# Performance work log

Measured on AMD Instinct MI355X. Metric: run time of the kernel, lower is better.

## Reference

```python
import jax, jax.numpy as jnp
import numpy as np

N, E, B = 40000, 640000, 256
F_IN, H, D = 128, 128, 128  # num_node_features, hidden_dim, last_dim
EPS = 1e-5


def sage_conv(x, src, dst, Wl, bl, Wr, num_nodes):
    # PyG SAGEConv (mean aggr): out = lin_l(mean_j x_j) + lin_r(x)
    msg = x[src]                                            # [E, d] gather
    agg = jax.ops.segment_sum(msg, dst, num_segments=num_nodes)
    cnt = jax.ops.segment_sum(jnp.ones((src.shape[0],), x.dtype), dst,
                              num_segments=num_nodes)
    mean = agg / jnp.maximum(cnt, 1.0)[:, None]
    return mean @ Wl.T + bl + x @ Wr.T


def bn_eval(x, g, b, rm, rv):
    return g * (x - rm) * jax.lax.rsqrt(rv + EPS) + b


def lstm_cell(inp, h, c, Wih, Whh, bih, bhh):
    gates = inp @ Wih.T + h @ Whh.T + bih + bhh             # [B, 4D]
    i, f, g, o = jnp.split(gates, 4, axis=-1)
    c = jax.nn.sigmoid(f) * c + jax.nn.sigmoid(i) * jnp.tanh(g)
    h = jax.nn.sigmoid(o) * jnp.tanh(c)
    return h, c


def set2set(x, batch, Wih, Whh, bih, bhh, num_graphs, steps=3):
    d = x.shape[1]
    q_star = jnp.zeros((num_graphs, 2 * d), x.dtype)
    h = jnp.zeros((num_graphs, d), x.dtype)
    c = jnp.zeros((num_graphs, d), x.dtype)
    for _ in range(steps):
        h, c = lstm_cell(q_star, h, c, Wih, Whh, bih, bhh)
        q = h                                               # [B, D]
        e = jnp.sum(x * q[batch], axis=-1)                  # [N]
        emax = jax.ops.segment_max(e, batch, num_segments=num_graphs)
        a = jnp.exp(e - emax[batch])
        denom = jax.ops.segment_sum(a, batch, num_segments=num_graphs)
        a = a / denom[batch]
        r = jax.ops.segment_sum(a[:, None] * x, batch, num_segments=num_graphs)
        q_star = jnp.concatenate([q, r], axis=-1)
    return q_star


def setup_inputs() -> dict:
    key = jax.random.key(0)
    ks = jax.random.split(key, 20)
    x = jax.random.normal(ks[0], (N, F_IN), jnp.float32)
    edge_index = jax.random.randint(ks[1], (2, E), 0, N)
    batch = jnp.sort(jax.random.randint(ks[2], (N,), 0, B))
    s1, s2, sd = 1.0 / np.sqrt(F_IN), 1.0 / np.sqrt(H), 1.0 / np.sqrt(D)
    return {
        "x": x, "edge_index": edge_index, "batch": batch,
        "W1l": jax.random.normal(ks[3], (H, F_IN)) * s1,
        "b1l": jnp.zeros((H,)),
        "W1r": jax.random.normal(ks[4], (H, F_IN)) * s1,
        "g1": jnp.ones((H,)), "beta1": jnp.zeros((H,)),
        "rm1": jax.random.normal(ks[5], (H,)) * 0.1,
        "rv1": jax.random.uniform(ks[6], (H,), minval=0.5, maxval=1.5),
        "W2l": jax.random.normal(ks[7], (D, H)) * s2,
        "b2l": jnp.zeros((D,)),
        "W2r": jax.random.normal(ks[8], (D, H)) * s2,
        "g2": jnp.ones((D,)), "beta2": jnp.zeros((D,)),
        "rm2": jax.random.normal(ks[9], (D,)) * 0.1,
        "rv2": jax.random.uniform(ks[10], (D,), minval=0.5, maxval=1.5),
        "Wih": jax.random.normal(ks[11], (4 * D, 2 * D)) * sd,
        "Whh": jax.random.normal(ks[12], (4 * D, D)) * sd,
        "bih": jnp.zeros((4 * D,)), "bhh": jnp.zeros((4 * D,)),
        "Wp": jax.random.normal(ks[13], (D, 2 * D)) * sd,
        "bp": jnp.zeros((D,)),
    }


def reference(x, edge_index, batch, W1l, b1l, W1r, g1, beta1, rm1, rv1,
              W2l, b2l, W2r, g2, beta2, rm2, rv2, Wih, Whh, bih, bhh, Wp, bp):
    src, dst = edge_index[0], edge_index[1]
    num_nodes = x.shape[0]
    h1 = jax.nn.relu(bn_eval(sage_conv(x, src, dst, W1l, b1l, W1r, num_nodes),
                             g1, beta1, rm1, rv1))
    # dropout is identity in eval mode
    h2 = jax.nn.relu(bn_eval(sage_conv(h1, src, dst, W2l, b2l, W2r, num_nodes),
                             g2, beta2, rm2, rv2))
    q_star = set2set(h2, batch, Wih, Whh, bih, bhh, B, steps=3)  # [B, 2D]
    return q_star @ Wp.T + bp                                    # [B, D]
```

## Files before the change

kernel.cpp:

```cpp
#include <hip/hip_runtime.h>
#include <hip/hip_bf16.h>
#include <math.h>

#define NN 40000
#define NE 640000
#define NG 256
#define FD 128
#define SLOT 96
#define NBK 1000
#define NPB 40
#define ECAP 832
#define BPAD 32

typedef __attribute__((ext_vector_type(8))) short bf16x8;
typedef __attribute__((ext_vector_type(4))) float f32x4;

__device__ __forceinline__ float sigf(float x) { return 1.f / (1.f + __expf(-x)); }
__device__ __forceinline__ unsigned short f2b(float f) {
    unsigned int u = __float_as_uint(f);
    return (unsigned short)((u + 0x7FFFu + ((u >> 16) & 1u)) >> 16);
}
__device__ __forceinline__ float b2f(unsigned int u16) {
    return __uint_as_float(u16 << 16);
}

__global__ __launch_bounds__(256) void k_fused1(
    const float* __restrict__ A,
    const float* __restrict__ W1l, const float* __restrict__ W1r,
    unsigned short* __restrict__ C,
    const int* __restrict__ ei, const int* __restrict__ batch,
    int* __restrict__ gptr, int* __restrict__ bcnt, unsigned int* __restrict__ ebuf,
    const float* __restrict__ W2l, const float* __restrict__ W2r,
    unsigned short* __restrict__ Wb,
    const float* __restrict__ Wihf, const float* __restrict__ Whhf,
    unsigned short* __restrict__ Wb2)
{
    __shared__ unsigned short Ws[128 * 128];
    int bid = blockIdx.x, t = threadIdx.x;

    if ((bid < 2012) && (bid & 1)) {
        int sidx = bid >> 1;
        if (sidx < 625) {
            int i = sidx * 256 + t;
            int4 s4 = ((const int4*)ei)[i];
            int4 d4 = ((const int4*)(ei + NE))[i];
            int b0 = d4.x / NPB;
            int p0 = atomicAdd(&bcnt[b0 * BPAD], 1);
            if (p0 < ECAP) ebuf[b0 * ECAP + p0] =
                (unsigned int)s4.x | ((unsigned int)(d4.x - b0 * NPB) << 16);
            int b1 = d4.y / NPB;
            int p1 = atomicAdd(&bcnt[b1 * BPAD], 1);
            if (p1 < ECAP) ebuf[b1 * ECAP + p1] =
                (unsigned int)s4.y | ((unsigned int)(d4.y - b1 * NPB) << 16);
            int b2 = d4.z / NPB;
            int p2 = atomicAdd(&bcnt[b2 * BPAD], 1);
            if (p2 < ECAP) ebuf[b2 * ECAP + p2] =
                (unsigned int)s4.z | ((unsigned int)(d4.z - b2 * NPB) << 16);
            int b3 = d4.w / NPB;
            int p3 = atomicAdd(&bcnt[b3 * BPAD], 1);
            if (p3 < ECAP) ebuf[b3 * ECAP + p3] =
                (unsigned int)s4.w | ((unsigned int)(d4.w - b3 * NPB) << 16);
        } else if (sidx < 782) {
            int i = (sidx - 625) * 256 + t;
            if (i >= NN) return;
            int b = batch[i];
            int pb = (i == 0) ? -1 : batch[i - 1];
            for (int g = pb + 1; g <= b; g++) gptr[g] = i;
            if (i == NN - 1)
                for (int g = b + 1; g <= NG; g++) gptr[g] = NN;
        } else if (sidx < 814) {
            int j4 = (sidx - 782) * 256 + t;
            int seg = j4 >> 12, off4 = j4 & 4095;
            const float* W = seg ? W2r : W2l;
            float4 v = ((const float4*)W)[off4];
            ushort4 o;
            o.x = f2b(v.x); o.y = f2b(v.y); o.z = f2b(v.z); o.w = f2b(v.w);
            *(ushort4*)(Wb + (size_t)j4 * 4) = o;
        } else {
            int j4 = (sidx - 814) * 256 + t;
            float4 v;
            size_t off;
            if (j4 < 32768) {
                int r = j4 >> 6, f4 = j4 & 63;
                int c = f4 >> 1, h = f4 & 1;
                v = ((const float4*)Wihf)[j4];
                off = ((size_t)c * 512 + r) * 8 + h * 4;
            } else {
                int jj = j4 - 32768;
                int r = jj >> 5, f4 = jj & 31;
                int c = f4 >> 1, h = f4 & 1;
                v = ((const float4*)Whhf)[jj];
                off = (size_t)512 * 256 + ((size_t)c * 512 + r) * 8 + h * 4;
            }
            ushort4 o;
            o.x = f2b(v.x); o.y = f2b(v.y); o.z = f2b(v.z); o.w = f2b(v.w);
            *(ushort4*)(Wb2 + off) = o;
        }
        return;
    }

    int mblk2 = (bid < 2012) ? (bid >> 1) : (bid - 1006);
    int nh = mblk2 & 1;
    int mblk = mblk2 >> 1;
    {
        const float* Wsrc = nh ? W1r : W1l;
#pragma unroll
        for (int i = 0; i < 8; i++) {
            int f = i * 256 + t;
            int row = f >> 4, c = f & 15;
            float4 u0 = *(const float4*)(Wsrc + row * 128 + c * 8);
            float4 u1 = *(const float4*)(Wsrc + row * 128 + c * 8 + 4);
            unsigned short tmp[8];
            tmp[0] = f2b(u0.x); tmp[1] = f2b(u0.y); tmp[2] = f2b(u0.z); tmp[3] = f2b(u0.w);
            tmp[4] = f2b(u1.x); tmp[5] = f2b(u1.y); tmp[6] = f2b(u1.z); tmp[7] = f2b(u1.w);
            int cs = c ^ (row & 15);
            *(uint4*)&Ws[row * 128 + cs * 8] = *(const uint4*)tmp;
        }
    }
    __syncthreads();
    int w = t >> 6, lane = t & 63;
    int ln = lane & 15, quad = lane >> 4;
    int m0 = mblk * 64 + w * 16;
    bf16x8 a[4];
    {
        const float* Arow = A + (size_t)(m0 + ln) * 128;
#pragma unroll
        for (int ks = 0; ks < 4; ks++) {
            float4 u0 = *(const float4*)(Arow + ks * 32 + quad * 8);
            float4 u1 = *(const float4*)(Arow + ks * 32 + quad * 8 + 4);
            unsigned short tmp[8];
            tmp[0] = f2b(u0.x); tmp[1] = f2b(u0.y); tmp[2] = f2b(u0.z); tmp[3] = f2b(u0.w);
            tmp[4] = f2b(u1.x); tmp[5] = f2b(u1.y); tmp[6] = f2b(u1.z); tmp[7] = f2b(u1.w);
            a[ks] = *(const bf16x8*)tmp;
        }
    }
    for (int nt = 0; nt < 8; nt++) {
        int n0 = nt * 16;
        int row = n0 + ln;
        f32x4 acc = {0.f, 0.f, 0.f, 0.f};
#pragma unroll
        for (int ks = 0; ks < 4; ks++) {
            int c = ks * 4 + quad;
            bf16x8 b = *(const bf16x8*)&Ws[row * 128 + (c ^ (row & 15)) * 8];
            acc = __builtin_amdgcn_mfma_f32_16x16x32_bf16(a[ks], b, acc, 0, 0, 0);
        }
        size_t base = (size_t)(m0 + quad * 4) * 256 + nh * 128 + n0 + ln;
#pragma unroll
        for (int r = 0; r < 4; r++)
            C[base + (size_t)r * 256] = f2b(acc[r]);
    }
}

__global__ __launch_bounds__(256) void k_mm_bf16(
    const unsigned short* __restrict__ A,
    const unsigned short* __restrict__ W,
    unsigned short* __restrict__ C)
{
    __shared__ unsigned short Ws[128 * 128];
    int t = threadIdx.x;
    int nh = blockIdx.x & 1;
    int mblk = blockIdx.x >> 1;
    {
        const uint4* Wg = (const uint4*)(W + nh * 128 * 128);
#pragma unroll
        for (int i = 0; i < 8; i++) {
            int f = i * 256 + t;
            int row = f >> 4, c = f & 15;
            int cs = c ^ (row & 15);
            *(uint4*)&Ws[row * 128 + cs * 8] = Wg[f];
        }
    }
    __syncthreads();
    int w = t >> 6, lane = t & 63;
    int ln = lane & 15, quad = lane >> 4;
    int m0 = mblk * 64 + w * 16;
    bf16x8 a[4];
    {
        const unsigned short* Arow = A + (size_t)(m0 + ln) * 128;
#pragma unroll
        for (int ks = 0; ks < 4; ks++)
            a[ks] = *(const bf16x8*)(Arow + ks * 32 + quad * 8);
    }
    for (int nt = 0; nt < 8; nt++) {
        int n0 = nt * 16;
        int row = n0 + ln;
        f32x4 acc = {0.f, 0.f, 0.f, 0.f};
#pragma unroll
        for (int ks = 0; ks < 4; ks++) {
            int c = ks * 4 + quad;
            bf16x8 b = *(const bf16x8*)&Ws[row * 128 + (c ^ (row & 15)) * 8];
            acc = __builtin_amdgcn_mfma_f32_16x16x32_bf16(a[ks], b, acc, 0, 0, 0);
        }
        size_t base = (size_t)(m0 + quad * 4) * 256 + nh * 128 + n0 + ln;
#pragma unroll
        for (int r = 0; r < 4; r++)
            C[base + (size_t)r * 256] = f2b(acc[r]);
    }
}

__global__ __launch_bounds__(256) void k_gather3(
    const unsigned short* __restrict__ C,
    const int* __restrict__ bcnt, const unsigned int* __restrict__ ebuf,
    const float* __restrict__ bl,
    const float* __restrict__ gam, const float* __restrict__ bet,
    const float* __restrict__ rme, const float* __restrict__ rva,
    unsigned short* __restrict__ H)
{
    __shared__ int lcnt[NPB];
    __shared__ int lsr[NPB][SLOT];
    int b = blockIdx.x, t = threadIdx.x;
    if (t < NPB) lcnt[t] = 0;
    __syncthreads();
    int cnt = bcnt[b * BPAD];
    if (cnt > ECAP) cnt = ECAP;
    for (int e = t; e < cnt; e += 256) {
        unsigned int u = ebuf[b * ECAP + e];
        int ld = u >> 16;
        int p = atomicAdd(&lcnt[ld], 1);
        if (p < SLOT) lsr[ld][p] = (int)(u & 0xFFFFu);
    }
    __syncthreads();

    int g = t >> 4, l4 = t & 15;
    const uint4* C4 = (const uint4*)C;

    float4 ga = ((const float4*)gam)[l4 * 2],     gb = ((const float4*)gam)[l4 * 2 + 1];
    float4 va = ((const float4*)rva)[l4 * 2],     vb = ((const float4*)rva)[l4 * 2 + 1];
    float4 ma = ((const float4*)rme)[l4 * 2],     mb = ((const float4*)rme)[l4 * 2 + 1];
    float4 ba = ((const float4*)bet)[l4 * 2],     bb = ((const float4*)bet)[l4 * 2 + 1];
    float4 la = ((const float4*)bl)[l4 * 2],      lb = ((const float4*)bl)[l4 * 2 + 1];
    float gq[8] = {ga.x, ga.y, ga.z, ga.w, gb.x, gb.y, gb.z, gb.w};
    float rv[8] = {va.x, va.y, va.z, va.w, vb.x, vb.y, vb.z, vb.w};
    float rm[8] = {ma.x, ma.y, ma.z, ma.w, mb.x, mb.y, mb.z, mb.w};
    float bt[8] = {ba.x, ba.y, ba.z, ba.w, bb.x, bb.y, bb.z, bb.w};
    float lv[8] = {la.x, la.y, la.z, la.w, lb.x, lb.y, lb.z, lb.w};

    for (int nd = g; nd < NPB; nd += 16) {
        int node = b * NPB + nd;
        int deg = lcnt[nd];
        int cn = (deg < SLOT) ? deg : SLOT;
        float ac[8];
#pragma unroll
        for (int k = 0; k < 8; k++) ac[k] = 0.f;
        int i = 0;
        for (; i + 7 < cn; i += 8) {
            uint4 v0 = C4[(size_t)lsr[nd][i]     * 32 + l4];
            uint4 v1 = C4[(size_t)lsr[nd][i + 1] * 32 + l4];
            uint4 v2 = C4[(size_t)lsr[nd][i + 2] * 32 + l4];
            uint4 v3 = C4[(size_t)lsr[nd][i + 3] * 32 + l4];
            uint4 v4 = C4[(size_t)lsr[nd][i + 4] * 32 + l4];
            uint4 v5 = C4[(size_t)lsr[nd][i + 5] * 32 + l4];
            uint4 v6 = C4[(size_t)lsr[nd][i + 6] * 32 + l4];
            uint4 v7 = C4[(size_t)lsr[nd][i + 7] * 32 + l4];
            ac[0] += b2f(v0.x & 0xFFFFu) + b2f(v1.x & 0xFFFFu) + b2f(v2.x & 0xFFFFu) + b2f(v3.x & 0xFFFFu)
                   + b2f(v4.x & 0xFFFFu) + b2f(v5.x & 0xFFFFu) + b2f(v6.x & 0xFFFFu) + b2f(v7.x & 0xFFFFu);
            ac[1] += b2f(v0.x >> 16) + b2f(v1.x >> 16) + b2f(v2.x >> 16) + b2f(v3.x >> 16)
                   + b2f(v4.x >> 16) + b2f(v5.x >> 16) + b2f(v6.x >> 16) + b2f(v7.x >> 16);
            ac[2] += b2f(v0.y & 0xFFFFu) + b2f(v1.y & 0xFFFFu) + b2f(v2.y & 0xFFFFu) + b2f(v3.y & 0xFFFFu)
                   + b2f(v4.y & 0xFFFFu) + b2f(v5.y & 0xFFFFu) + b2f(v6.y & 0xFFFFu) + b2f(v7.y & 0xFFFFu);
            ac[3] += b2f(v0.y >> 16) + b2f(v1.y >> 16) + b2f(v2.y >> 16) + b2f(v3.y >> 16)
                   + b2f(v4.y >> 16) + b2f(v5.y >> 16) + b2f(v6.y >> 16) + b2f(v7.y >> 16);
            ac[4] += b2f(v0.z & 0xFFFFu) + b2f(v1.z & 0xFFFFu) + b2f(v2.z & 0xFFFFu) + b2f(v3.z & 0xFFFFu)
                   + b2f(v4.z & 0xFFFFu) + b2f(v5.z & 0xFFFFu) + b2f(v6.z & 0xFFFFu) + b2f(v7.z & 0xFFFFu);
            ac[5] += b2f(v0.z >> 16) + b2f(v1.z >> 16) + b2f(v2.z >> 16) + b2f(v3.z >> 16)
                   + b2f(v4.z >> 16) + b2f(v5.z >> 16) + b2f(v6.z >> 16) + b2f(v7.z >> 16);
            ac[6] += b2f(v0.w & 0xFFFFu) + b2f(v1.w & 0xFFFFu) + b2f(v2.w & 0xFFFFu) + b2f(v3.w & 0xFFFFu)
                   + b2f(v4.w & 0xFFFFu) + b2f(v5.w & 0xFFFFu) + b2f(v6.w & 0xFFFFu) + b2f(v7.w & 0xFFFFu);
            ac[7] += b2f(v0.w >> 16) + b2f(v1.w >> 16) + b2f(v2.w >> 16) + b2f(v3.w >> 16)
                   + b2f(v4.w >> 16) + b2f(v5.w >> 16) + b2f(v6.w >> 16) + b2f(v7.w >> 16);
        }
        for (; i < cn; i++) {
            uint4 v = C4[(size_t)lsr[nd][i] * 32 + l4];
            ac[0] += b2f(v.x & 0xFFFFu); ac[1] += b2f(v.x >> 16);
            ac[2] += b2f(v.y & 0xFFFFu); ac[3] += b2f(v.y >> 16);
            ac[4] += b2f(v.z & 0xFFFFu); ac[5] += b2f(v.z >> 16);
            ac[6] += b2f(v.w & 0xFFFFu); ac[7] += b2f(v.w >> 16);
        }
        float inv = 1.0f / fmaxf((float)deg, 1.0f);
        uint4 yr = C4[(size_t)node * 32 + 16 + l4];
        float yo[8];
        yo[0] = b2f(yr.x & 0xFFFFu); yo[1] = b2f(yr.x >> 16);
        yo[2] = b2f(yr.y & 0xFFFFu); yo[3] = b2f(yr.y >> 16);
        yo[4] = b2f(yr.z & 0xFFFFu); yo[5] = b2f(yr.z >> 16);
        yo[6] = b2f(yr.w & 0xFFFFu); yo[7] = b2f(yr.w >> 16);
        unsigned short o[8];
#pragma unroll
        for (int k = 0; k < 8; k++) {
            float y = ac[k] * inv + yo[k] + lv[k];
            float z = gq[k] * rsqrtf(rv[k] + 1e-5f) * (y - rm[k]) + bt[k];
            o[k] = f2b(fmaxf(z, 0.f));
        }
        *(uint4*)(H + (size_t)node * 128 + l4 * 8) = *(const uint4*)o;
    }
}

__global__ __launch_bounds__(1024) void k_s2s(
    const unsigned short* __restrict__ h2, const int* __restrict__ gptr,
    const float* __restrict__ bih, const float* __restrict__ bhh,
    const unsigned short* __restrict__ Wihb, const unsigned short* __restrict__ Whhb,
    const float* __restrict__ Wp, const float* __restrict__ bp,
    float* __restrict__ out)
{
    int b = blockIdx.x, t = threadIdx.x;
    int wave = t >> 6, lane = t & 63;
    int grp = t >> 4, l4 = t & 15;
    __shared__ float hs[FD];
    __shared__ float qstar[2 * FD];
    __shared__ float gates_s[512];
    __shared__ float es[512];
    __shared__ float wm[16], wd[16], red[16][FD];
    float creg = 0.f;
    int start = gptr[b], end = gptr[b + 1];
    int seg = end - start;
    const unsigned int* H2 = (const unsigned int*)h2;
    const uint4* H4 = (const uint4*)h2;

    for (int step = 0; step < 3; step++) {
        if (step == 0) {
            if (t < FD) {
                float ig = bih[t] + bhh[t];
                float gg = bih[2 * FD + t] + bhh[2 * FD + t];
                float og = bih[3 * FD + t] + bhh[3 * FD + t];
                float c = sigf(ig) * tanhf(gg);
                float h = sigf(og) * tanhf(c);
                creg = c; hs[t] = h;
            }
        } else {
            if (t < 512) {
                float acc = bih[t] + bhh[t];
                const uint4* wi = (const uint4*)Wihb;
                for (int k = 0; k < 32; k++) {
                    uint4 u = wi[k * 512 + t];
                    const float* q = &qstar[k * 8];
                    acc += b2f(u.x & 0xFFFFu)*q[0] + b2f(u.x >> 16)*q[1]
                         + b2f(u.y & 0xFFFFu)*q[2] + b2f(u.y >> 16)*q[3]
                         + b2f(u.z & 0xFFFFu)*q[4] + b2f(u.z >> 16)*q[5]
                         + b2f(u.w & 0xFFFFu)*q[6] + b2f(u.w >> 16)*q[7];
                }
                const uint4* wh = (const uint4*)Whhb;
                for (int k = 0; k < 16; k++) {
                    uint4 u = wh[k * 512 + t];
                    const float* hq = &hs[k * 8];
                    acc += b2f(u.x & 0xFFFFu)*hq[0] + b2f(u.x >> 16)*hq[1]
                         + b2f(u.y & 0xFFFFu)*hq[2] + b2f(u.y >> 16)*hq[3]
                         + b2f(u.z & 0xFFFFu)*hq[4] + b2f(u.z >> 16)*hq[5]
                         + b2f(u.w & 0xFFFFu)*hq[6] + b2f(u.w >> 16)*hq[7];
                }
                gates_s[t] = acc;
            }
            __syncthreads();
            if (t < FD) {
                float ig = gates_s[t], fg = gates_s[FD + t];
                float gg = gates_s[2 * FD + t], og = gates_s[3 * FD + t];
                float c = sigf(fg) * creg + sigf(ig) * tanhf(gg);
                float h = sigf(og) * tanhf(c);
                creg = c; hs[t] = h;
            }
        }
        __syncthreads();

        if (seg <= 512) {
            float4 qa = ((const float4*)hs)[l4 * 2];
            float4 qb = ((const float4*)hs)[l4 * 2 + 1];
            float mg = -INFINITY;
            for (int n = start + grp; n < end; n += 64) {
                uint4 v = H4[(size_t)n * 16 + l4];
                float e = qa.x * b2f(v.x & 0xFFFFu) + qa.y * b2f(v.x >> 16)
                        + qa.z * b2f(v.y & 0xFFFFu) + qa.w * b2f(v.y >> 16)
                        + qb.x * b2f(v.z & 0xFFFFu) + qb.y * b2f(v.z >> 16)
                        + qb.z * b2f(v.w & 0xFFFFu) + qb.w * b2f(v.w >> 16);
#pragma unroll
                for (int off = 8; off; off >>= 1) e += __shfl_xor(e, off);
                if (l4 == 0) es[n - start] = e;
                mg = fmaxf(mg, e);
            }
            mg = fmaxf(mg, __shfl_xor(mg, 16));
            mg = fmaxf(mg, __shfl_xor(mg, 32));
            if (lane == 0) wm[wave] = mg;
            __syncthreads();
            float M = wm[0];
#pragma unroll
            for (int k = 1; k < 16; k++) M = fmaxf(M, wm[k]);
            float r8[8];
#pragma unroll
            for (int j = 0; j < 8; j++) r8[j] = 0.f;
            float dwl = 0.f;
            for (int n = start + grp; n < end; n += 64) {
                uint4 v = H4[(size_t)n * 16 + l4];
                float a = __expf(es[n - start] - M);
                r8[0] += a * b2f(v.x & 0xFFFFu); r8[1] += a * b2f(v.x >> 16);
                r8[2] += a * b2f(v.y & 0xFFFFu); r8[3] += a * b2f(v.y >> 16);
                r8[4] += a * b2f(v.z & 0xFFFFu); r8[5] += a * b2f(v.z >> 16);
                r8[6] += a * b2f(v.w & 0xFFFFu); r8[7] += a * b2f(v.w >> 16);
                dwl += a;
            }
#pragma unroll
            for (int j = 0; j < 8; j++) {
                r8[j] += __shfl_xor(r8[j], 16);
                r8[j] += __shfl_xor(r8[j], 32);
            }
            dwl += __shfl_xor(dwl, 16);
            dwl += __shfl_xor(dwl, 32);
            if (lane < 16) {
                float4 wa = {r8[0], r8[1], r8[2], r8[3]};
                float4 wb = {r8[4], r8[5], r8[6], r8[7]};
                *(float4*)&red[wave][lane * 8]     = wa;
                *(float4*)&red[wave][lane * 8 + 4] = wb;
            }
            if (lane == 0) wd[wave] = dwl;
        } else {
            float2 q = ((const float2*)hs)[lane];
            float rx = 0.f, ry = 0.f, dw = 0.f;
            float mw = -INFINITY;
            for (int n = start + wave; n < end; n += 16) {
                unsigned int u = H2[(size_t)n * 64 + lane];
                float vx = b2f(u & 0xFFFFu), vy = b2f(u >> 16);
                float e = vx * q.x + vy * q.y;
#pragma unroll
                for (int off = 32; off; off >>= 1) e += __shfl_xor(e, off);
                float mn = fmaxf(mw, e);
                float corr = __expf(mw - mn);
                float a = __expf(e - mn);
                rx = rx * corr + a * vx;
                ry = ry * corr + a * vy;
                dw = dw * corr + a;
                mw = mn;
            }
            if (lane == 0) wm[wave] = mw;
            __syncthreads();
            float M = wm[0];
#pragma unroll
            for (int k = 1; k < 16; k++) M = fmaxf(M, wm[k]);
            float cr = (M == -INFINITY) ? 0.f : __expf(mw - M);
            red[wave][2 * lane] = rx * cr;
            red[wave][2 * lane + 1] = ry * cr;
            if (lane == 0) wd[wave] = dw * cr;
        }
        __syncthreads();
        if (t < FD) {
            float r = 0.f, den = 0.f;
#pragma unroll
            for (int k = 0; k < 16; k++) { r += red[k][t]; den += wd[k]; }
            float rn = (den > 0.f) ? r / den : 0.f;
            qstar[t] = hs[t];
            qstar[FD + t] = rn;
        }
        __syncthreads();
    }

    if (t < FD) {
        const float4* w4 = (const float4*)(Wp + (size_t)t * 256);
        const float4* q4 = (const float4*)qstar;
        float acc = bp[t];
        for (int k = 0; k < 64; k++) {
            float4 wv = w4[k], qv = q4[k];
            acc += qv.x*wv.x + qv.y*wv.y + qv.z*wv.z + qv.w*wv.w;
        }
        out[(size_t)b * FD + t] = acc;
    }
}

__global__ void k_zero_out(float* __restrict__ out, int n) {
    int i = blockIdx.x * blockDim.x + threadIdx.x;
    if (i < n) out[i] = 0.f;
}

extern "C" void kernel_launch(void* const* d_in, const int* in_sizes, int n_in,
                              void* d_out, int out_size, void* d_ws, size_t ws_size,
                              hipStream_t stream) {
    const float* x   = (const float*)d_in[0];
    const int*  ei    = (const int*)d_in[1];
    const int*  batch = (const int*)d_in[2];
    const float* W1l = (const float*)d_in[3];
    const float* b1l = (const float*)d_in[4];
    const float* W1r = (const float*)d_in[5];
    const float* g1  = (const float*)d_in[6];
    const float* be1 = (const float*)d_in[7];
    const float* rm1 = (const float*)d_in[8];
    const float* rv1 = (const float*)d_in[9];
    const float* W2l = (const float*)d_in[10];
    const float* b2l = (const float*)d_in[11];
    const float* W2r = (const float*)d_in[12];
    const float* g2  = (const float*)d_in[13];
    const float* be2 = (const float*)d_in[14];
    const float* rm2 = (const float*)d_in[15];
    const float* rv2 = (const float*)d_in[16];
    const float* Wih = (const float*)d_in[17];
    const float* Whh = (const float*)d_in[18];
    const float* bih = (const float*)d_in[19];
    const float* bhh = (const float*)d_in[20];
    const float* Wp  = (const float*)d_in[21];
    const float* bp  = (const float*)d_in[22];
    float* out = (float*)d_out;

    auto al = [](size_t s) { return (s + 255) & ~(size_t)255; };
    size_t off_bcnt = 0;
    size_t off_ebuf = off_bcnt + al((size_t)NBK * BPAD * 4);
    size_t off_gptr = off_ebuf + al((size_t)NBK * ECAP * 4);
    size_t off_h2b  = off_gptr + al((size_t)(NG + 1) * 4);
    size_t off_h1b  = off_h2b  + al((size_t)NN * FD * 2);
    size_t off_Wb   = off_h1b  + al((size_t)NN * FD * 2);
    size_t off_Wb2  = off_Wb   + al((size_t)256 * 128 * 2);
    size_t off_C    = off_Wb2  + al((size_t)(512 * 256 + 512 * 128) * 2);
    size_t need     = off_C    + al((size_t)NN * 256 * 2);

    if (ws_size < need) {
        k_zero_out<<<(out_size + 255) / 256, 256, 0, stream>>>(out, out_size);
        return;
    }

    char* p = (char*)d_ws;
    int* bcnt    = (int*)(p + off_bcnt);
    unsigned int* ebuf = (unsigned int*)(p + off_ebuf);
    int* gptr    = (int*)(p + off_gptr);
    unsigned short* h2b = (unsigned short*)(p + off_h2b);
    unsigned short* h1b = (unsigned short*)(p + off_h1b);
    unsigned short* Wb  = (unsigned short*)(p + off_Wb);
    unsigned short* Wb2 = (unsigned short*)(p + off_Wb2);
    unsigned short* C   = (unsigned short*)(p + off_C);

    hipMemsetAsync(bcnt, 0, (size_t)NBK * BPAD * 4, stream);

    k_fused1<<<2256, 256, 0, stream>>>(x, W1l, W1r, C,
                                       ei, batch, gptr, bcnt, ebuf,
                                       W2l, W2r, Wb, Wih, Whh, Wb2);
    k_gather3<<<NBK, 256, 0, stream>>>(C, bcnt, ebuf, b1l, g1, be1, rm1, rv1, h1b);

    k_mm_bf16<<<1250, 256, 0, stream>>>(h1b, Wb, C);
    k_gather3<<<NBK, 256, 0, stream>>>(C, bcnt, ebuf, b2l, g2, be2, rm2, rv2, h2b);

    k_s2s<<<NG, 1024, 0, stream>>>(h2b, gptr, bih, bhh,
                                   Wb2, Wb2 + 512 * 256, Wp, bp, out);
}
```

Baseline: 228.4 us.

## Fuse layer-2 neighbor mean aggregation with its linear transforms and batchnorm

Layer 2 previously ran a separate GEMM producing both projections (lin_l and lin_r) for all nodes, then gathered the projected rows. The new kernel first aggregates raw h1 rows per node into shared memory, then applies the lin_l and lin_r weights with MFMA, followed by bias, batchnorm and ReLU, all in one kernel. This removes one launch and the write and read of the 40000x256 intermediate C. In exchange, each block reloads the weight fragments per column tile, and the mean is rounded to bf16 before the matmul, which changes the numerics slightly.

```diff
diff --git a/kernel.cpp b/kernel.cpp
--- a/kernel.cpp
+++ b/kernel.cpp
@@ -151,53 +151,6 @@
     }
 }
 
-__global__ __launch_bounds__(256) void k_mm_bf16(
-    const unsigned short* __restrict__ A,
-    const unsigned short* __restrict__ W,
-    unsigned short* __restrict__ C)
-{
-    __shared__ unsigned short Ws[128 * 128];
-    int t = threadIdx.x;
-    int nh = blockIdx.x & 1;
-    int mblk = blockIdx.x >> 1;
-    {
-        const uint4* Wg = (const uint4*)(W + nh * 128 * 128);
-#pragma unroll
-        for (int i = 0; i < 8; i++) {
-            int f = i * 256 + t;
-            int row = f >> 4, c = f & 15;
-            int cs = c ^ (row & 15);
-            *(uint4*)&Ws[row * 128 + cs * 8] = Wg[f];
-        }
-    }
-    __syncthreads();
-    int w = t >> 6, lane = t & 63;
-    int ln = lane & 15, quad = lane >> 4;
-    int m0 = mblk * 64 + w * 16;
-    bf16x8 a[4];
-    {
-        const unsigned short* Arow = A + (size_t)(m0 + ln) * 128;
-#pragma unroll
-        for (int ks = 0; ks < 4; ks++)
-            a[ks] = *(const bf16x8*)(Arow + ks * 32 + quad * 8);
-    }
-    for (int nt = 0; nt < 8; nt++) {
-        int n0 = nt * 16;
-        int row = n0 + ln;
-        f32x4 acc = {0.f, 0.f, 0.f, 0.f};
-#pragma unroll
-        for (int ks = 0; ks < 4; ks++) {
-            int c = ks * 4 + quad;
-            bf16x8 b = *(const bf16x8*)&Ws[row * 128 + (c ^ (row & 15)) * 8];
-            acc = __builtin_amdgcn_mfma_f32_16x16x32_bf16(a[ks], b, acc, 0, 0, 0);
-        }
-        size_t base = (size_t)(m0 + quad * 4) * 256 + nh * 128 + n0 + ln;
-#pragma unroll
-        for (int r = 0; r < 4; r++)
-            C[base + (size_t)r * 256] = f2b(acc[r]);
-    }
-}
-
 __global__ __launch_bounds__(256) void k_gather3(
     const unsigned short* __restrict__ C,
     const int* __restrict__ bcnt, const unsigned int* __restrict__ ebuf,
@@ -294,6 +247,132 @@
     }
 }
 
+__global__ __launch_bounds__(256) void k_gather_l2(
+    const unsigned short* __restrict__ h1,
+    const int* __restrict__ bcnt, const unsigned int* __restrict__ ebuf,
+    const unsigned short* __restrict__ Wb,
+    const float* __restrict__ bl,
+    const float* __restrict__ gam, const float* __restrict__ bet,
+    const float* __restrict__ rme, const float* __restrict__ rva,
+    unsigned short* __restrict__ H2)
+{
+    __shared__ int lcnt[NPB];
+    __shared__ unsigned short lsr[NPB][SLOT];
+    __shared__ unsigned short ms[48 * 128];
+    int b = blockIdx.x, t = threadIdx.x;
+    if (t < NPB) lcnt[t] = 0;
+    if (t < 128) {
+        int r = 40 + (t >> 4), cpos = t & 15;
+        uint4 zz; zz.x = zz.y = zz.z = zz.w = 0u;
+        *(uint4*)&ms[r * 128 + cpos * 8] = zz;
+    }
+    __syncthreads();
+    int cnt = bcnt[b * BPAD];
+    if (cnt > ECAP) cnt = ECAP;
+    for (int e = t; e < cnt; e += 256) {
+        unsigned int u = ebuf[b * ECAP + e];
+        int ld = u >> 16;
+        int p = atomicAdd(&lcnt[ld], 1);
+        if (p < SLOT) lsr[ld][p] = (unsigned short)(u & 0xFFFFu);
+    }
+    __syncthreads();
+
+    int g = t >> 4, l4 = t & 15;
+    const uint4* H14 = (const uint4*)h1;
+
+    for (int nd = g; nd < NPB; nd += 16) {
+        int deg = lcnt[nd];
+        int cn = (deg < SLOT) ? deg : SLOT;
+        float ac[8];
+#pragma unroll
+        for (int k = 0; k < 8; k++) ac[k] = 0.f;
+        int i = 0;
+        for (; i + 7 < cn; i += 8) {
+            uint4 v0 = H14[(size_t)lsr[nd][i]     * 16 + l4];
+            uint4 v1 = H14[(size_t)lsr[nd][i + 1] * 16 + l4];
+            uint4 v2 = H14[(size_t)lsr[nd][i + 2] * 16 + l4];
+            uint4 v3 = H14[(size_t)lsr[nd][i + 3] * 16 + l4];
+            uint4 v4 = H14[(size_t)lsr[nd][i + 4] * 16 + l4];
+            uint4 v5 = H14[(size_t)lsr[nd][i + 5] * 16 + l4];
+            uint4 v6 = H14[(size_t)lsr[nd][i + 6] * 16 + l4];
+            uint4 v7 = H14[(size_t)lsr[nd][i + 7] * 16 + l4];
+            ac[0] += b2f(v0.x & 0xFFFFu) + b2f(v1.x & 0xFFFFu) + b2f(v2.x & 0xFFFFu) + b2f(v3.x & 0xFFFFu)
+                   + b2f(v4.x & 0xFFFFu) + b2f(v5.x & 0xFFFFu) + b2f(v6.x & 0xFFFFu) + b2f(v7.x & 0xFFFFu);
+            ac[1] += b2f(v0.x >> 16) + b2f(v1.x >> 16) + b2f(v2.x >> 16) + b2f(v3.x >> 16)
+                   + b2f(v4.x >> 16) + b2f(v5.x >> 16) + b2f(v6.x >> 16) + b2f(v7.x >> 16);
+            ac[2] += b2f(v0.y & 0xFFFFu) + b2f(v1.y & 0xFFFFu) + b2f(v2.y & 0xFFFFu) + b2f(v3.y & 0xFFFFu)
+                   + b2f(v4.y & 0xFFFFu) + b2f(v5.y & 0xFFFFu) + b2f(v6.y & 0xFFFFu) + b2f(v7.y & 0xFFFFu);
+            ac[3] += b2f(v0.y >> 16) + b2f(v1.y >> 16) + b2f(v2.y >> 16) + b2f(v3.y >> 16)
+                   + b2f(v4.y >> 16) + b2f(v5.y >> 16) + b2f(v6.y >> 16) + b2f(v7.y >> 16);
+            ac[4] += b2f(v0.z & 0xFFFFu) + b2f(v1.z & 0xFFFFu) + b2f(v2.z & 0xFFFFu) + b2f(v3.z & 0xFFFFu)
+                   + b2f(v4.z & 0xFFFFu) + b2f(v5.z & 0xFFFFu) + b2f(v6.z & 0xFFFFu) + b2f(v7.z & 0xFFFFu);
+            ac[5] += b2f(v0.z >> 16) + b2f(v1.z >> 16) + b2f(v2.z >> 16) + b2f(v3.z >> 16)
+                   + b2f(v4.z >> 16) + b2f(v5.z >> 16) + b2f(v6.z >> 16) + b2f(v7.z >> 16);
+            ac[6] += b2f(v0.w & 0xFFFFu) + b2f(v1.w & 0xFFFFu) + b2f(v2.w & 0xFFFFu) + b2f(v3.w & 0xFFFFu)
+                   + b2f(v4.w & 0xFFFFu) + b2f(v5.w & 0xFFFFu) + b2f(v6.w & 0xFFFFu) + b2f(v7.w & 0xFFFFu);
+            ac[7] += b2f(v0.w >> 16) + b2f(v1.w >> 16) + b2f(v2.w >> 16) + b2f(v3.w >> 16)
+                   + b2f(v4.w >> 16) + b2f(v5.w >> 16) + b2f(v6.w >> 16) + b2f(v7.w >> 16);
+        }
+        for (; i < cn; i++) {
+            uint4 v = H14[(size_t)lsr[nd][i] * 16 + l4];
+            ac[0] += b2f(v.x & 0xFFFFu); ac[1] += b2f(v.x >> 16);
+            ac[2] += b2f(v.y & 0xFFFFu); ac[3] += b2f(v.y >> 16);
+            ac[4] += b2f(v.z & 0xFFFFu); ac[5] += b2f(v.z >> 16);
+            ac[6] += b2f(v.w & 0xFFFFu); ac[7] += b2f(v.w >> 16);
+        }
+        float inv = 1.0f / fmaxf((float)deg, 1.0f);
+        unsigned short mo[8];
+#pragma unroll
+        for (int k = 0; k < 8; k++) mo[k] = f2b(ac[k] * inv);
+        *(uint4*)&ms[nd * 128 + ((l4 ^ (nd & 15)) * 8)] = *(const uint4*)mo;
+    }
+    __syncthreads();
+
+    int w = t >> 6, lane = t & 63;
+    int ln = lane & 15, quad = lane >> 4;
+    int node0 = b * NPB;
+    for (int nt = w; nt < 8; nt += 4) {
+        int n0 = nt * 16;
+        int col = n0 + ln;
+        bf16x8 bfr[8];
+#pragma unroll
+        for (int ks = 0; ks < 8; ks++) {
+            int wrow = (ks < 4) ? col : (128 + col);
+            int c = (ks & 3) * 4 + quad;
+            bfr[ks] = *(const bf16x8*)(Wb + wrow * 128 + c * 8);
+        }
+        float bcol  = bl[col];
+        float sc    = gam[col] * rsqrtf(rva[col] + 1e-5f);
+        float mcol  = rme[col], becol = bet[col];
+        for (int m0 = 0; m0 < 48; m0 += 16) {
+            int arow = m0 + ln;
+            f32x4 acc = {0.f, 0.f, 0.f, 0.f};
+#pragma unroll
+            for (int ks = 0; ks < 4; ks++) {
+                int c = ks * 4 + quad;
+                bf16x8 a = *(const bf16x8*)&ms[arow * 128 + ((c ^ (arow & 15)) * 8)];
+                acc = __builtin_amdgcn_mfma_f32_16x16x32_bf16(a, bfr[ks], acc, 0, 0, 0);
+            }
+            int selfrow = node0 + arow;
+            if (selfrow >= NN) selfrow = NN - 1;
+#pragma unroll
+            for (int ks = 0; ks < 4; ks++) {
+                bf16x8 a = *(const bf16x8*)(h1 + (size_t)selfrow * 128 + ks * 32 + quad * 8);
+                acc = __builtin_amdgcn_mfma_f32_16x16x32_bf16(a, bfr[4 + ks], acc, 0, 0, 0);
+            }
+#pragma unroll
+            for (int r = 0; r < 4; r++) {
+                int row = m0 + quad * 4 + r;
+                if (row < NPB) {
+                    float y = acc[r] + bcol;
+                    float z = sc * (y - mcol) + becol;
+                    H2[(size_t)(node0 + row) * 128 + col] = f2b(fmaxf(z, 0.f));
+                }
+            }
+        }
+    }
+}
+
 __global__ __launch_bounds__(1024) void k_s2s(
     const unsigned short* __restrict__ h2, const int* __restrict__ gptr,
     const float* __restrict__ bih, const float* __restrict__ bhh,
@@ -526,8 +605,8 @@
                                        W2l, W2r, Wb, Wih, Whh, Wb2);
     k_gather3<<<NBK, 256, 0, stream>>>(C, bcnt, ebuf, b1l, g1, be1, rm1, rv1, h1b);
 
-    k_mm_bf16<<<1250, 256, 0, stream>>>(h1b, Wb, C);
-    k_gather3<<<NBK, 256, 0, stream>>>(C, bcnt, ebuf, b2l, g2, be2, rm2, rv2, h2b);
+    k_gather_l2<<<NBK, 256, 0, stream>>>(h1b, bcnt, ebuf, Wb,
+                                         b2l, g2, be2, rm2, rv2, h2b);
 
     k_s2s<<<NG, 1024, 0, stream>>>(h2b, gptr, bih, bhh,
                                    Wb2, Wb2 + 512 * 256, Wp, bp, out);
```

New measurement: 237.9 us. 1.04x slower.
